# Optimization experiments

Measured on AMD Instinct MI355X. Metric: run time of the kernel, lower is better.

## Reference

```python
import jax, jax.numpy as jnp
import numpy as np

B, Hh, Ww, E = 8, 32, 32, 256
HEADS = 8
KD = E // HEADS  # 32
FFN = 1024
NQ = 64
SCALING = KD ** -0.5
EPS = 1e-6


def _ln(x, g, b):
    m = x.mean(-1, keepdims=True)
    v = ((x - m) ** 2).mean(-1, keepdims=True)
    return (x - m) * jax.lax.rsqrt(v + EPS) * g + b


def _dwconv(x, w, b, pad):
    # x: (b,h,w,c); w: (c,1,kh,kw) depthwise
    y = jnp.transpose(x, (0, 3, 1, 2))
    y = jax.lax.conv_general_dilated(
        y, w, (1, 1), [(pad, pad), (pad, pad)],
        dimension_numbers=('NCHW', 'OIHW', 'NCHW'),
        feature_group_count=y.shape[1])
    y = y + b[None, :, None, None]
    return jnp.transpose(y, (0, 2, 3, 1))


def _rot2(x):
    x1 = x[..., ::2]
    x2 = x[..., 1::2]
    return jnp.stack([-x2, x1], axis=-1).reshape(x.shape)


def _theta_shift(x, sin, cos):
    return x * cos + _rot2(x) * sin


def _ffn(x, fc1_w, fc1_b, fc2_w, fc2_b):
    h = jax.nn.gelu(x @ fc1_w.T + fc1_b, approximate=False)
    return h @ fc2_w.T + fc2_b


def _mha(q, k, v, in_w, in_b, out_w, out_b):
    # torch nn.MultiheadAttention, batch_first=True
    wq, wk, wv = in_w[:E], in_w[E:2 * E], in_w[2 * E:]
    bq, bk, bv = in_b[:E], in_b[E:2 * E], in_b[2 * E:]
    b_, nq, _ = q.shape
    lk = k.shape[1]
    qp = (q @ wq.T + bq).reshape(b_, nq, HEADS, KD).transpose(0, 2, 1, 3)
    kp = (k @ wk.T + bk).reshape(b_, lk, HEADS, KD).transpose(0, 2, 1, 3)
    vp = (v @ wv.T + bv).reshape(b_, lk, HEADS, KD).transpose(0, 2, 1, 3)
    att = jax.nn.softmax(jnp.einsum('bhqd,bhkd->bhqk', qp, kp) * SCALING, axis=-1)
    out = jnp.einsum('bhqk,bhkd->bhqd', att, vp)
    out = out.transpose(0, 2, 1, 3).reshape(b_, nq, E)
    return out @ out_w.T + out_b


def setup_inputs() -> dict:
    key = jax.random.key(0)
    ks = jax.random.split(key, 24)
    n = lambda i, shp, s=1.0: jax.random.normal(ks[i], shp, jnp.float32) * s
    W = 0.02
    return {
        'x': n(0, (B, Hh, Ww, E)),
        'queries': n(1, (B, NQ, E)),
        'sin': n(2, (Hh, Ww, KD)),
        'cos': n(3, (Hh, Ww, KD)),
        'mask': n(4, (HEADS, Hh * Ww, Hh * Ww)),
        'ln1_g': jnp.ones((E,), jnp.float32), 'ln1_b': jnp.zeros((E,), jnp.float32),
        'ln2_g': jnp.ones((E,), jnp.float32), 'ln2_b': jnp.zeros((E,), jnp.float32),
        'wq': n(5, (E, E), W), 'bq': jnp.zeros((E,), jnp.float32),
        'wk': n(6, (E, E), W), 'bk': jnp.zeros((E,), jnp.float32),
        'wv': n(7, (E, E), W), 'bv': jnp.zeros((E,), jnp.float32),
        'lepe_w': n(8, (E, 1, 5, 5), W), 'lepe_b': jnp.zeros((E,), jnp.float32),
        'wo': n(9, (E, E), W), 'bo': jnp.zeros((E,), jnp.float32),
        'fc1_w': n(10, (FFN, E), W), 'fc1_b': jnp.zeros((FFN,), jnp.float32),
        'fc2_w': n(11, (E, FFN), W), 'fc2_b': jnp.zeros((E,), jnp.float32),
        'pos_w': n(12, (E, 1, 3, 3), W), 'pos_b': jnp.zeros((E,), jnp.float32),
        'ca_in_w': n(13, (3 * E, E), W), 'ca_in_b': jnp.zeros((3 * E,), jnp.float32),
        'ca_out_w': n(14, (E, E), W), 'ca_out_b': jnp.zeros((E,), jnp.float32),
    }


def reference(x, queries, sin, cos, mask, ln1_g, ln1_b, ln2_g, ln2_b,
              wq, bq, wk, bk, wv, bv, lepe_w, lepe_b, wo, bo,
              fc1_w, fc1_b, fc2_w, fc2_b, pos_w, pos_b,
              ca_in_w, ca_in_b, ca_out_w, ca_out_b):
    # conditional positional encoding
    x = x + _dwconv(x, pos_w, pos_b, 1)

    # --- retention branch (VisionRetentionAll) ---
    hn = _ln(x, ln1_g, ln1_b)
    q = hn @ wq.T + bq
    k = (hn @ wk.T + bk) * SCALING
    v = hn @ wv.T + bv
    lepe = _dwconv(v, lepe_w, lepe_b, 2)
    b_, hh, ww, _ = x.shape
    L = hh * ww
    qh = q.reshape(b_, hh, ww, HEADS, KD).transpose(0, 3, 1, 2, 4)
    kh = k.reshape(b_, hh, ww, HEADS, KD).transpose(0, 3, 1, 2, 4)
    qr = _theta_shift(qh, sin, cos).reshape(b_, HEADS, L, KD)
    kr = _theta_shift(kh, sin, cos).reshape(b_, HEADS, L, KD)
    vr = v.reshape(b_, hh, ww, HEADS, KD).transpose(0, 3, 1, 2, 4).reshape(b_, HEADS, L, KD)
    att = jax.nn.softmax(jnp.einsum('bnqd,bnkd->bnqk', qr, kr) + mask, axis=-1)
    out = jnp.einsum('bnqk,bnkd->bnqd', att, vr)
    out = out.transpose(0, 2, 1, 3).reshape(b_, hh, ww, E) + lepe
    x = x + (out @ wo.T + bo)

    # --- FFN branch ---
    x = x + _ffn(_ln(x, ln2_g, ln2_b), fc1_w, fc1_b, fc2_w, fc2_b)

    # --- cross-attention on queries ---
    xs = x.reshape(b_, L, E)
    q_ln = _ln(queries, ln1_g, ln1_b)
    queries = queries + _mha(q_ln, xs, xs, ca_in_w, ca_in_b, ca_out_w, ca_out_b)
    queries = queries + _ffn(_ln(queries, ln2_g, ln2_b), fc1_w, fc1_b, fc2_w, fc2_b)
    return x, queries
```

## Files before the change

kernel.cpp:

```cpp
#include <hip/hip_runtime.h>
#include <hip/hip_bf16.h>

#define B_      8
#define HH      32
#define WW      32
#define E_      256
#define HEADS_  8
#define KD_     32
#define FFN_    1024
#define NQ_     64
#define L_      1024
#define SCALING_ 0.17677669529663687f
#define EPS_    1e-6f

typedef short bf16x8 __attribute__((ext_vector_type(8)));
typedef float f32x4 __attribute__((ext_vector_type(4)));
typedef unsigned short ushort_t;

__device__ __forceinline__ ushort_t f2bf(float f) {
    __hip_bfloat16 h = __float2bfloat16(f);
    return *reinterpret_cast<ushort_t*>(&h);
}
__device__ __forceinline__ float bf2f(ushort_t u) {
    __hip_bfloat16 h = *reinterpret_cast<__hip_bfloat16*>(&u);
    return __bfloat162float(h);
}

__global__ void dwT_kernel(const float* __restrict__ lepe_w, const float* __restrict__ pos_w,
                           float* __restrict__ LWT, float* __restrict__ PWT) {
    int e = threadIdx.x;
#pragma unroll
    for (int t = 0; t < 25; ++t) LWT[t * 256 + e] = lepe_w[e * 25 + t];
#pragma unroll
    for (int t = 0; t < 9; ++t) PWT[t * 256 + e] = pos_w[e * 9 + t];
}

__global__ __launch_bounds__(256) void posconv_ln2(
        const float* __restrict__ x, const float* __restrict__ PWT,
        const float* __restrict__ bias, const float* __restrict__ g,
        const float* __restrict__ bb, float* __restrict__ X, ushort_t* __restrict__ HN) {
    int tid = threadIdx.x;
    int wave = tid >> 6, lane = tid & 63;
    int b = blockIdx.x >> 8, rem = blockIdx.x & 255;
    int hh = rem >> 3, wg = rem & 7;
    int ww = wg * 4 + wave;
    int e = lane * 4;
    long row = ((long)(b * HH + hh)) * WW + ww;

    float4 bi = *reinterpret_cast<const float4*>(bias + e);
    float ax = bi.x, ay = bi.y, az = bi.z, aw = bi.w;
#pragma unroll
    for (int dh = 0; dh < 3; ++dh) {
        int h2 = hh + dh - 1; if (h2 < 0 || h2 >= HH) continue;
        float rx = 0.f, ry = 0.f, rz = 0.f, rw = 0.f;
#pragma unroll
        for (int dw = 0; dw < 3; ++dw) {
            int w2 = ww + dw - 1; if (w2 < 0 || w2 >= WW) continue;
            float4 v = *reinterpret_cast<const float4*>(x + (((long)(b * HH + h2)) * WW + w2) * E_ + e);
            float4 wt = *reinterpret_cast<const float4*>(PWT + (dh * 3 + dw) * 256 + e);
            rx += v.x * wt.x; ry += v.y * wt.y; rz += v.z * wt.z; rw += v.w * wt.w;
        }
        ax += rx; ay += ry; az += rz; aw += rw;
    }
    float4 x4 = *reinterpret_cast<const float4*>(x + row * E_ + e);
    float vx = x4.x + ax, vy = x4.y + ay, vz = x4.z + az, vw = x4.w + aw;
    float4 o4 = {vx, vy, vz, vw};
    *reinterpret_cast<float4*>(X + row * E_ + e) = o4;

    float s = vx + vy + vz + vw;
#pragma unroll
    for (int off = 1; off < 64; off <<= 1) s += __shfl_xor(s, off);
    float mean = s * (1.0f / E_);
    float dx = vx - mean, dy = vy - mean, dz = vz - mean, dw_ = vw - mean;
    float s2 = dx * dx + dy * dy + dz * dz + dw_ * dw_;
#pragma unroll
    for (int off = 1; off < 64; off <<= 1) s2 += __shfl_xor(s2, off);
    float r = rsqrtf(s2 * (1.0f / E_) + EPS_);
    float4 g4 = *reinterpret_cast<const float4*>(g + e);
    float4 b4 = *reinterpret_cast<const float4*>(bb + e);
    uint2 p;
    p.x = (unsigned int)f2bf(dx * r * g4.x + b4.x) | ((unsigned int)f2bf(dy * r * g4.y + b4.y) << 16);
    p.y = (unsigned int)f2bf(dz * r * g4.z + b4.z) | ((unsigned int)f2bf(dw_ * r * g4.w + b4.w) << 16);
    *reinterpret_cast<uint2*>(HN + row * E_ + e) = p;
}

__global__ __launch_bounds__(256) void lepe2(
        const float* __restrict__ v, const float* __restrict__ LWT,
        const float* __restrict__ bias, float* __restrict__ out) {
    int tid = threadIdx.x;
    int wave = tid >> 6, lane = tid & 63;
    int b = blockIdx.x >> 8, rem = blockIdx.x & 255;
    int hh = rem >> 3, wg = rem & 7;
    int ww = wg * 4 + wave;
    int e = lane * 4;
    long row = ((long)(b * HH + hh)) * WW + ww;

    float4 bi = *reinterpret_cast<const float4*>(bias + e);
    float ax = bi.x, ay = bi.y, az = bi.z, aw = bi.w;
#pragma unroll
    for (int dh = 0; dh < 5; ++dh) {
        int h2 = hh + dh - 2; if (h2 < 0 || h2 >= HH) continue;
        float rx = 0.f, ry = 0.f, rz = 0.f, rw = 0.f;
#pragma unroll
        for (int dw = 0; dw < 5; ++dw) {
            int w2 = ww + dw - 2; if (w2 < 0 || w2 >= WW) continue;
            float4 vv = *reinterpret_cast<const float4*>(v + (((long)(b * HH + h2)) * WW + w2) * E_ + e);
            float4 wt = *reinterpret_cast<const float4*>(LWT + (dh * 5 + dw) * 256 + e);
            rx += vv.x * wt.x; ry += vv.y * wt.y; rz += vv.z * wt.z; rw += vv.w * wt.w;
        }
        ax += rx; ay += ry; az += rz; aw += rw;
    }
    float4 o4 = {ax, ay, az, aw};
    *reinterpret_cast<float4*>(out + row * E_ + e) = o4;
}

__global__ __launch_bounds__(256) void ln2(
        const float* __restrict__ x, const float* __restrict__ g,
        const float* __restrict__ b, ushort_t* __restrict__ y) {
    int tid = threadIdx.x;
    int wave = tid >> 6, lane = tid & 63;
    long row = (long)blockIdx.x * 4 + wave;
    int e = lane * 4;
    float4 v4 = *reinterpret_cast<const float4*>(x + row * E_ + e);
    float s = v4.x + v4.y + v4.z + v4.w;
#pragma unroll
    for (int off = 1; off < 64; off <<= 1) s += __shfl_xor(s, off);
    float mean = s * (1.0f / E_);
    float dx = v4.x - mean, dy = v4.y - mean, dz = v4.z - mean, dw = v4.w - mean;
    float s2 = dx * dx + dy * dy + dz * dz + dw * dw;
#pragma unroll
    for (int off = 1; off < 64; off <<= 1) s2 += __shfl_xor(s2, off);
    float r = rsqrtf(s2 * (1.0f / E_) + EPS_);
    float4 g4 = *reinterpret_cast<const float4*>(g + e);
    float4 b4 = *reinterpret_cast<const float4*>(b + e);
    uint2 p;
    p.x = (unsigned int)f2bf(dx * r * g4.x + b4.x) | ((unsigned int)f2bf(dy * r * g4.y + b4.y) << 16);
    p.y = (unsigned int)f2bf(dz * r * g4.z + b4.z) | ((unsigned int)f2bf(dw * r * g4.w + b4.w) << 16);
    *reinterpret_cast<uint2*>(y + row * E_ + e) = p;
}

__global__ void maskcvt_kernel(const float* __restrict__ m, ushort_t* __restrict__ o) {
    long i = ((long)blockIdx.x * 256 + threadIdx.x) * 4;
    float4 v = *reinterpret_cast<const float4*>(m + i);
    uint2 p;
    p.x = (unsigned int)f2bf(v.x) | ((unsigned int)f2bf(v.y) << 16);
    p.y = (unsigned int)f2bf(v.z) | ((unsigned int)f2bf(v.w) << 16);
    *reinterpret_cast<uint2*>(o + i) = p;
}

struct WTab { const float* src[8]; };
__global__ void wconv_kernel(WTab t, ushort_t* __restrict__ dst) {
    const int off[9] = {0, 65536, 131072, 196608, 262144, 524288, 786432, 983040, 1048576};
    long base = ((long)blockIdx.x * 256 + threadIdx.x) * 4;
    int r = 0;
#pragma unroll
    for (int i = 1; i < 8; ++i) r = (base >= off[i]) ? i : r;
    const float* s =
        r == 0 ? t.src[0] : r == 1 ? t.src[1] : r == 2 ? t.src[2] : r == 3 ? t.src[3] :
        r == 4 ? t.src[4] : r == 5 ? t.src[5] : r == 6 ? t.src[6] : t.src[7];
    float4 v = *reinterpret_cast<const float4*>(s + (base - off[r]));
    uint2 p;
    p.x = (unsigned int)f2bf(v.x) | ((unsigned int)f2bf(v.y) << 16);
    p.y = (unsigned int)f2bf(v.z) | ((unsigned int)f2bf(v.w) << 16);
    *reinterpret_cast<uint2*>(dst + base) = p;
}

template<int ACT, int THETA>
__global__ __launch_bounds__(256) void gemm2(
        const ushort_t* __restrict__ A, const ushort_t* __restrict__ W,
        const float* __restrict__ bias, ushort_t* __restrict__ Cb,
        float* __restrict__ Cf, const float* __restrict__ resid,
        int M, int N, int K, float scale, int scaleN,
        const float* __restrict__ sinp, const float* __restrict__ cosp) {
    __shared__ __align__(16) ushort_t As[64 * 72];
    __shared__ __align__(16) ushort_t Ws[64 * 72];
    int tid = threadIdx.x;
    int wave = tid >> 6, lane = tid & 63;
    int quad = lane >> 4, l16 = lane & 15;
    int wm = wave >> 1, wn = wave & 1;
    long mBase = (long)blockIdx.x * 64;
    long nBase = (long)blockIdx.y * 64;
    int row = tid >> 3, q = tid & 7;
    int row2 = (tid + 256) >> 3, q2 = (tid + 256) & 7;

    f32x4 acc[2][2];
#pragma unroll
    for (int i = 0; i < 2; ++i)
#pragma unroll
        for (int j = 0; j < 2; ++j) acc[i][j] = (f32x4){0.f, 0.f, 0.f, 0.f};

    int nT = K >> 6;
    uint4 a0 = *reinterpret_cast<const uint4*>(A + (mBase + row) * (long)K + q * 8);
    uint4 a1 = *reinterpret_cast<const uint4*>(A + (mBase + row2) * (long)K + q2 * 8);
    uint4 w0 = *reinterpret_cast<const uint4*>(W + (nBase + row) * (long)K + q * 8);
    uint4 w1 = *reinterpret_cast<const uint4*>(W + (nBase + row2) * (long)K + q2 * 8);

    for (int t = 0; t < nT; ++t) {
        *reinterpret_cast<uint4*>(&As[row * 72 + q * 8]) = a0;
        *reinterpret_cast<uint4*>(&As[row2 * 72 + q2 * 8]) = a1;
        *reinterpret_cast<uint4*>(&Ws[row * 72 + q * 8]) = w0;
        *reinterpret_cast<uint4*>(&Ws[row2 * 72 + q2 * 8]) = w1;
        __syncthreads();
        if (t + 1 < nT) {
            int kt = (t + 1) << 6;
            a0 = *reinterpret_cast<const uint4*>(A + (mBase + row) * (long)K + kt + q * 8);
            a1 = *reinterpret_cast<const uint4*>(A + (mBase + row2) * (long)K + kt + q2 * 8);
            w0 = *reinterpret_cast<const uint4*>(W + (nBase + row) * (long)K + kt + q * 8);
            w1 = *reinterpret_cast<const uint4*>(W + (nBase + row2) * (long)K + kt + q2 * 8);
        }
#pragma unroll
        for (int kk = 0; kk < 2; ++kk) {
            bf16x8 af[2], bfr[2];
#pragma unroll
            for (int i = 0; i < 2; ++i)
                af[i] = *reinterpret_cast<const bf16x8*>(&As[(wm * 32 + i * 16 + l16) * 72 + kk * 32 + quad * 8]);
#pragma unroll
            for (int j = 0; j < 2; ++j)
                bfr[j] = *reinterpret_cast<const bf16x8*>(&Ws[(wn * 32 + j * 16 + l16) * 72 + kk * 32 + quad * 8]);
#pragma unroll
            for (int i = 0; i < 2; ++i)
#pragma unroll
                for (int j = 0; j < 2; ++j)
                    acc[i][j] = __builtin_amdgcn_mfma_f32_16x16x32_bf16(af[i], bfr[j], acc[i][j], 0, 0, 0);
        }
        __syncthreads();
    }

#pragma unroll
    for (int i = 0; i < 2; ++i)
#pragma unroll
        for (int j = 0; j < 2; ++j) {
            long n = nBase + wn * 32 + j * 16 + l16;
            float bn = bias[n];
            float eff = (n < scaleN) ? scale : 1.0f;
#pragma unroll
            for (int r = 0; r < 4; ++r) {
                long m = mBase + wm * 32 + i * 16 + quad * 4 + r;
                float v = (acc[i][j][r] + bn) * eff;
                if (THETA) {
                    float other = __shfl_xor(v, 1);
                    int l = (int)(m & (L_ - 1));
                    int d = (int)(n & 31);
                    float cc = cosp[l * 32 + d], ss = sinp[l * 32 + d];
                    v = v * cc + ((n & 1) ? other : -other) * ss;
                }
                if (ACT) v = 0.5f * v * (1.0f + erff(v * 0.70710678118654752f));
                if (resid) v += resid[m * N + n];
                if (Cf) Cf[m * N + n] = v;
                if (Cb) Cb[m * N + n] = f2bf(v);
            }
        }
}

__global__ __launch_bounds__(256) void attn3(
        const ushort_t* __restrict__ Q, int qs,
        const ushort_t* __restrict__ K, int ks,
        const ushort_t* __restrict__ V, int vs,
        const ushort_t* __restrict__ maskbf,
        const float* __restrict__ lepe, ushort_t* __restrict__ out, int nq) {
    __shared__ __align__(16) ushort_t Vt[2][32 * 136];
    __shared__ __align__(16) ushort_t Pl[4][16 * 136];
    int tid = threadIdx.x;
    int wave = tid >> 6, lane = tid & 63;
    int quad = lane >> 4, l16 = lane & 15;
    int qt = blockIdx.x, h = blockIdx.y, b = blockIdx.z;
    int qbase = qt * 64 + wave * 16;

    bf16x8 qfrag = *reinterpret_cast<const bf16x8*>(
        Q + ((long)b * nq + qbase + l16) * qs + h * KD_ + quad * 8);

    f32x4 acc_o[2];
    acc_o[0] = (f32x4){0.f, 0.f, 0.f, 0.f};
    acc_o[1] = (f32x4){0.f, 0.f, 0.f, 0.f};
    float lsum[4] = {0.f, 0.f, 0.f, 0.f};

    int kp = tid & 63;
    int dq = tid >> 6;

    const ushort_t* vp = V + ((long)b * L_ + 2 * kp) * vs + h * KD_ + dq * 8;
    uint4 ua = *reinterpret_cast<const uint4*>(vp);
    uint4 ub = *reinterpret_cast<const uint4*>(vp + vs);
    {
        const unsigned int* wa = reinterpret_cast<const unsigned int*>(&ua);
        const unsigned int* wb = reinterpret_cast<const unsigned int*>(&ub);
#pragma unroll
        for (int i = 0; i < 8; ++i) {
            unsigned int x16 = (wa[i >> 1] >> ((i & 1) * 16)) & 0xFFFF;
            unsigned int y16 = (wb[i >> 1] >> ((i & 1) * 16)) & 0xFFFF;
            *reinterpret_cast<unsigned int*>(&Vt[0][(dq * 8 + i) * 136 + 2 * kp]) =
                x16 | (y16 << 16);
        }
    }

    for (int it = 0; it < 8; ++it) {
        int kb = it * 128;
        __syncthreads();
        if (it < 7) {
            const ushort_t* vn = V + ((long)b * L_ + kb + 128 + 2 * kp) * vs + h * KD_ + dq * 8;
            ua = *reinterpret_cast<const uint4*>(vn);
            ub = *reinterpret_cast<const uint4*>(vn + vs);
        }

#pragma unroll
        for (int g = 0; g < 2; ++g) {
            bf16x8 kf[4];
#pragma unroll
            for (int kt = 0; kt < 4; ++kt)
                kf[kt] = *reinterpret_cast<const bf16x8*>(
                    K + ((long)b * L_ + kb + (g * 4 + kt) * 16 + l16) * ks + h * KD_ + quad * 8);
#pragma unroll
            for (int kt = 0; kt < 4; ++kt) {
                int kcol = (g * 4 + kt) * 16;
                f32x4 sa;
                if (maskbf) {
#pragma unroll
                    for (int r = 0; r < 4; ++r)
                        sa[r] = bf2f(maskbf[((long)h * L_ + qbase + quad * 4 + r) * L_ + kb + kcol + l16]);
                } else {
                    sa = (f32x4){0.f, 0.f, 0.f, 0.f};
                }
                sa = __builtin_amdgcn_mfma_f32_16x16x32_bf16(qfrag, kf[kt], sa, 0, 0, 0);
#pragma unroll
                for (int r = 0; r < 4; ++r) {
                    float p = __expf(sa[r]);
                    lsum[r] += p;
                    Pl[wave][(quad * 4 + r) * 136 + kcol + l16] = f2bf(p);
                }
            }
        }

#pragma unroll
        for (int c = 0; c < 4; ++c) {
            bf16x8 pa = *reinterpret_cast<const bf16x8*>(
                &Pl[wave][l16 * 136 + c * 32 + quad * 8]);
#pragma unroll
            for (int dt = 0; dt < 2; ++dt) {
                bf16x8 vf = *reinterpret_cast<const bf16x8*>(
                    &Vt[it & 1][(dt * 16 + l16) * 136 + c * 32 + quad * 8]);
                acc_o[dt] = __builtin_amdgcn_mfma_f32_16x16x32_bf16(pa, vf, acc_o[dt], 0, 0, 0);
            }
        }

        if (it < 7) {
            const unsigned int* wa = reinterpret_cast<const unsigned int*>(&ua);
            const unsigned int* wb = reinterpret_cast<const unsigned int*>(&ub);
#pragma unroll
            for (int i = 0; i < 8; ++i) {
                unsigned int x16 = (wa[i >> 1] >> ((i & 1) * 16)) & 0xFFFF;
                unsigned int y16 = (wb[i >> 1] >> ((i & 1) * 16)) & 0xFFFF;
                *reinterpret_cast<unsigned int*>(&Vt[(it + 1) & 1][(dq * 8 + i) * 136 + 2 * kp]) =
                    x16 | (y16 << 16);
            }
        }
    }

#pragma unroll
    for (int off = 1; off < 16; off <<= 1) {
#pragma unroll
        for (int r = 0; r < 4; ++r) lsum[r] += __shfl_xor(lsum[r], off);
    }

#pragma unroll
    for (int dt = 0; dt < 2; ++dt)
#pragma unroll
        for (int r = 0; r < 4; ++r) {
            float v = acc_o[dt][r] / lsum[r];
            long oi = ((long)b * nq + qbase + quad * 4 + r) * E_ + h * KD_ + dt * 16 + l16;
            if (lepe) v += lepe[oi];
            out[oi] = f2bf(v);
        }
}

extern "C" void kernel_launch(void* const* d_in, const int* in_sizes, int n_in,
                              void* d_out, int out_size, void* d_ws, size_t ws_size,
                              hipStream_t stream) {
    const float* x        = (const float*)d_in[0];
    const float* queries  = (const float*)d_in[1];
    const float* sinp     = (const float*)d_in[2];
    const float* cosp     = (const float*)d_in[3];
    const float* mask     = (const float*)d_in[4];
    const float* ln1_g    = (const float*)d_in[5];
    const float* ln1_b    = (const float*)d_in[6];
    const float* ln2_g    = (const float*)d_in[7];
    const float* ln2_b    = (const float*)d_in[8];
    const float* wq       = (const float*)d_in[9];
    const float* bq       = (const float*)d_in[10];
    const float* wk       = (const float*)d_in[11];
    const float* bk       = (const float*)d_in[12];
    const float* wv       = (const float*)d_in[13];
    const float* bv       = (const float*)d_in[14];
    const float* lepe_w   = (const float*)d_in[15];
    const float* lepe_b   = (const float*)d_in[16];
    const float* wo       = (const float*)d_in[17];
    const float* bo       = (const float*)d_in[18];
    const float* fc1_w    = (const float*)d_in[19];
    const float* fc1_b    = (const float*)d_in[20];
    const float* fc2_w    = (const float*)d_in[21];
    const float* fc2_b    = (const float*)d_in[22];
    const float* pos_w    = (const float*)d_in[23];
    const float* pos_b    = (const float*)d_in[24];
    const float* ca_in_w  = (const float*)d_in[25];
    const float* ca_in_b  = (const float*)d_in[26];
    const float* ca_out_w = (const float*)d_in[27];
    const float* ca_out_b = (const float*)d_in[28];

    float* ws = (float*)d_ws;
    const long SZ = (long)B_ * L_ * E_;
    float* X    = ws;
    float* Vbf  = ws + SZ;
    float* LEP  = ws + 2 * SZ;
    float* Q2   = LEP;
    ushort_t* U = (ushort_t*)(ws + 3 * SZ);
    ushort_t* T0    = U;
    ushort_t* Qb_u  = U + SZ;
    ushort_t* Kb_u  = U + 2 * SZ;
    ushort_t* Vb_u  = U + 3 * SZ;
    ushort_t* HID_u = U + 4 * SZ;
    ushort_t* MB_u  = HID_u;
    ushort_t* WB    = U + 8 * SZ;
    float* LWT      = (float*)(WB + 1048576);
    float* PWT      = LWT + 6400;
    ushort_t* KV_u   = U + SZ;
    ushort_t* QLN_u  = Vb_u;
    ushort_t* QP_u   = Vb_u + 131072;
    ushort_t* CAO_u  = Vb_u + 262144;
    ushort_t* QHID_u = Vb_u + 393216;
    ushort_t* wqB    = WB;
    ushort_t* wkB    = WB + 65536;
    ushort_t* wvB    = WB + 131072;
    ushort_t* woB    = WB + 196608;
    ushort_t* fc1B   = WB + 262144;
    ushort_t* fc2B   = WB + 524288;
    ushort_t* cainB  = WB + 786432;
    ushort_t* caoutB = WB + 983040;

    float* XOUT = (float*)d_out;
    float* QOUT = (float*)d_out + 2097152;

    dim3 blk(256);
    const int rows = B_ * L_;
    const float* Z = nullptr;

    WTab wt;
    wt.src[0] = wq; wt.src[1] = wk; wt.src[2] = wv; wt.src[3] = wo;
    wt.src[4] = fc1_w; wt.src[5] = fc2_w; wt.src[6] = ca_in_w; wt.src[7] = ca_out_w;

    dwT_kernel<<<1, blk, 0, stream>>>(lepe_w, pos_w, LWT, PWT);
    wconv_kernel<<<1024, blk, 0, stream>>>(wt, WB);
    maskcvt_kernel<<<8192, blk, 0, stream>>>(mask, MB_u);
    posconv_ln2<<<2048, blk, 0, stream>>>(x, PWT, pos_b, ln1_g, ln1_b, X, T0);

    gemm2<0,1><<<dim3(128, 4), blk, 0, stream>>>(T0, wqB, bq, Qb_u, nullptr, Z, rows, 256, 256, 1.0f, 0, sinp, cosp);
    gemm2<0,1><<<dim3(128, 4), blk, 0, stream>>>(T0, wkB, bk, Kb_u, nullptr, Z, rows, 256, 256, SCALING_, 256, sinp, cosp);
    gemm2<0,0><<<dim3(128, 4), blk, 0, stream>>>(T0, wvB, bv, Vb_u, Vbf, Z, rows, 256, 256, 1.0f, 0, Z, Z);
    lepe2<<<2048, blk, 0, stream>>>(Vbf, LWT, lepe_b, LEP);
    attn3<<<dim3(16, 8, 8), blk, 0, stream>>>(Qb_u, 256, Kb_u, 256, Vb_u, 256, MB_u, LEP, T0, L_);
    gemm2<0,0><<<dim3(128, 4), blk, 0, stream>>>(T0, woB, bo, nullptr, X, X, rows, 256, 256, 1.0f, 0, Z, Z);
    ln2<<<2048, blk, 0, stream>>>(X, ln2_g, ln2_b, T0);
    gemm2<1,0><<<dim3(128, 16), blk, 0, stream>>>(T0, fc1B, fc1_b, HID_u, nullptr, Z, rows, 1024, 256, 1.0f, 0, Z, Z);
    gemm2<0,0><<<dim3(128, 4), blk, 0, stream>>>(HID_u, fc2B, fc2_b, T0, XOUT, X, rows, 256, 1024, 1.0f, 0, Z, Z);

    ln2<<<128, blk, 0, stream>>>(queries, ln1_g, ln1_b, QLN_u);
    gemm2<0,0><<<dim3(8, 4), blk, 0, stream>>>(QLN_u, cainB, ca_in_b, QP_u, nullptr, Z, 512, 256, 256, 1.0f, 0, Z, Z);
    gemm2<0,0><<<dim3(128, 8), blk, 0, stream>>>(T0, cainB + 65536, ca_in_b + 256, KV_u, nullptr, Z, rows, 512, 256, SCALING_, 256, Z, Z);
    attn3<<<dim3(1, 8, 8), blk, 0, stream>>>(QP_u, 256, KV_u, 512, KV_u + 256, 512, nullptr, nullptr, CAO_u, NQ_);
    gemm2<0,0><<<dim3(8, 4), blk, 0, stream>>>(CAO_u, caoutB, ca_out_b, nullptr, Q2, queries, 512, 256, 256, 1.0f, 0, Z, Z);
    ln2<<<128, blk, 0, stream>>>(Q2, ln2_g, ln2_b, QLN_u);
    gemm2<1,0><<<dim3(8, 16), blk, 0, stream>>>(QLN_u, fc1B, fc1_b, QHID_u, nullptr, Z, 512, 1024, 256, 1.0f, 0, Z, Z);
    gemm2<0,0><<<dim3(8, 4), blk, 0, stream>>>(QHID_u, fc2B, fc2_b, nullptr, QOUT, Q2, 512, 256, 1024, 1.0f, 0, Z, Z);
}
```

Before: 367.3 us.

## Fold log2e into K scale and mask, use exp2 and transposed score MFMA

The log2(e) factor is folded into the key scaling and the bf16 mask conversion, so softmax can use the native exp2 instead of expf. The score MFMA swaps its operands, so each lane holds four consecutive keys of one query row. This allows vectorized mask loads preloaded into registers, packed bf16 stores of P to LDS, and a single running sum per lane reduced with fewer shuffles. Float-to-bf16 packing also moves to a paired conversion helper everywhere. The mask now stores pre-scaled values, which changes bf16 rounding slightly and raises register use for the preloaded mask.

```diff
diff --git a/kernel.cpp b/kernel.cpp
--- a/kernel.cpp
+++ b/kernel.cpp
@@ -11,19 +11,26 @@
 #define NQ_     64
 #define L_      1024
 #define SCALING_ 0.17677669529663687f
+#define LOG2E_  1.44269504088896340736f
 #define EPS_    1e-6f
 
 typedef short bf16x8 __attribute__((ext_vector_type(8)));
 typedef float f32x4 __attribute__((ext_vector_type(4)));
 typedef unsigned short ushort_t;
 
+#if __has_builtin(__builtin_amdgcn_exp2f)
+#define EXP2(x) __builtin_amdgcn_exp2f(x)
+#else
+#define EXP2(x) exp2f(x)
+#endif
+
 __device__ __forceinline__ ushort_t f2bf(float f) {
     __hip_bfloat16 h = __float2bfloat16(f);
     return *reinterpret_cast<ushort_t*>(&h);
 }
-__device__ __forceinline__ float bf2f(ushort_t u) {
-    __hip_bfloat16 h = *reinterpret_cast<__hip_bfloat16*>(&u);
-    return __bfloat162float(h);
+__device__ __forceinline__ unsigned int pk2(float a, float b) {
+    __hip_bfloat162 h = __float22bfloat162_rn(float2{a, b});
+    return *reinterpret_cast<unsigned int*>(&h);
 }
 
 __global__ void dwT_kernel(const float* __restrict__ lepe_w, const float* __restrict__ pos_w,
@@ -79,8 +86,8 @@
     float4 g4 = *reinterpret_cast<const float4*>(g + e);
     float4 b4 = *reinterpret_cast<const float4*>(bb + e);
     uint2 p;
-    p.x = (unsigned int)f2bf(dx * r * g4.x + b4.x) | ((unsigned int)f2bf(dy * r * g4.y + b4.y) << 16);
-    p.y = (unsigned int)f2bf(dz * r * g4.z + b4.z) | ((unsigned int)f2bf(dw_ * r * g4.w + b4.w) << 16);
+    p.x = pk2(dx * r * g4.x + b4.x, dy * r * g4.y + b4.y);
+    p.y = pk2(dz * r * g4.z + b4.z, dw_ * r * g4.w + b4.w);
     *reinterpret_cast<uint2*>(HN + row * E_ + e) = p;
 }
 
@@ -134,8 +141,8 @@
     float4 g4 = *reinterpret_cast<const float4*>(g + e);
     float4 b4 = *reinterpret_cast<const float4*>(b + e);
     uint2 p;
-    p.x = (unsigned int)f2bf(dx * r * g4.x + b4.x) | ((unsigned int)f2bf(dy * r * g4.y + b4.y) << 16);
-    p.y = (unsigned int)f2bf(dz * r * g4.z + b4.z) | ((unsigned int)f2bf(dw * r * g4.w + b4.w) << 16);
+    p.x = pk2(dx * r * g4.x + b4.x, dy * r * g4.y + b4.y);
+    p.y = pk2(dz * r * g4.z + b4.z, dw * r * g4.w + b4.w);
     *reinterpret_cast<uint2*>(y + row * E_ + e) = p;
 }
 
@@ -143,8 +150,8 @@
     long i = ((long)blockIdx.x * 256 + threadIdx.x) * 4;
     float4 v = *reinterpret_cast<const float4*>(m + i);
     uint2 p;
-    p.x = (unsigned int)f2bf(v.x) | ((unsigned int)f2bf(v.y) << 16);
-    p.y = (unsigned int)f2bf(v.z) | ((unsigned int)f2bf(v.w) << 16);
+    p.x = pk2(v.x * LOG2E_, v.y * LOG2E_);
+    p.y = pk2(v.z * LOG2E_, v.w * LOG2E_);
     *reinterpret_cast<uint2*>(o + i) = p;
 }
 
@@ -160,8 +167,8 @@
         r == 4 ? t.src[4] : r == 5 ? t.src[5] : r == 6 ? t.src[6] : t.src[7];
     float4 v = *reinterpret_cast<const float4*>(s + (base - off[r]));
     uint2 p;
-    p.x = (unsigned int)f2bf(v.x) | ((unsigned int)f2bf(v.y) << 16);
-    p.y = (unsigned int)f2bf(v.z) | ((unsigned int)f2bf(v.w) << 16);
+    p.x = pk2(v.x, v.y);
+    p.y = pk2(v.z, v.w);
     *reinterpret_cast<uint2*>(dst + base) = p;
 }
 
@@ -252,7 +259,7 @@
         }
 }
 
-__global__ __launch_bounds__(256) void attn3(
+__global__ __launch_bounds__(256) void attn4(
         const ushort_t* __restrict__ Q, int qs,
         const ushort_t* __restrict__ K, int ks,
         const ushort_t* __restrict__ V, int vs,
@@ -272,7 +279,7 @@
     f32x4 acc_o[2];
     acc_o[0] = (f32x4){0.f, 0.f, 0.f, 0.f};
     acc_o[1] = (f32x4){0.f, 0.f, 0.f, 0.f};
-    float lsum[4] = {0.f, 0.f, 0.f, 0.f};
+    float lsum = 0.f;
 
     int kp = tid & 63;
     int dq = tid >> 6;
@@ -300,32 +307,39 @@
             ua = *reinterpret_cast<const uint4*>(vn);
             ub = *reinterpret_cast<const uint4*>(vn + vs);
         }
+        uint2 mreg[8];
+        if (maskbf) {
+            const ushort_t* mb = maskbf + ((long)h * L_ + qbase + l16) * L_ + kb + quad * 4;
+#pragma unroll
+            for (int kt = 0; kt < 8; ++kt)
+                mreg[kt] = *reinterpret_cast<const uint2*>(mb + kt * 16);
+        }
 
 #pragma unroll
         for (int g = 0; g < 2; ++g) {
             bf16x8 kf[4];
 #pragma unroll
-            for (int kt = 0; kt < 4; ++kt)
-                kf[kt] = *reinterpret_cast<const bf16x8*>(
-                    K + ((long)b * L_ + kb + (g * 4 + kt) * 16 + l16) * ks + h * KD_ + quad * 8);
-#pragma unroll
-            for (int kt = 0; kt < 4; ++kt) {
-                int kcol = (g * 4 + kt) * 16;
-                f32x4 sa;
+            for (int kt4 = 0; kt4 < 4; ++kt4)
+                kf[kt4] = *reinterpret_cast<const bf16x8*>(
+                    K + ((long)b * L_ + kb + (g * 4 + kt4) * 16 + l16) * ks + h * KD_ + quad * 8);
+#pragma unroll
+            for (int kt4 = 0; kt4 < 4; ++kt4) {
+                int kt = g * 4 + kt4;
+                f32x4 sa = (f32x4){0.f, 0.f, 0.f, 0.f};
+                sa = __builtin_amdgcn_mfma_f32_16x16x32_bf16(kf[kt4], qfrag, sa, 0, 0, 0);
+                float s0 = sa[0], s1 = sa[1], s2 = sa[2], s3 = sa[3];
                 if (maskbf) {
-#pragma unroll
-                    for (int r = 0; r < 4; ++r)
-                        sa[r] = bf2f(maskbf[((long)h * L_ + qbase + quad * 4 + r) * L_ + kb + kcol + l16]);
-                } else {
-                    sa = (f32x4){0.f, 0.f, 0.f, 0.f};
+                    s0 += __uint_as_float(mreg[kt].x << 16);
+                    s1 += __uint_as_float(mreg[kt].x & 0xFFFF0000u);
+                    s2 += __uint_as_float(mreg[kt].y << 16);
+                    s3 += __uint_as_float(mreg[kt].y & 0xFFFF0000u);
                 }
-                sa = __builtin_amdgcn_mfma_f32_16x16x32_bf16(qfrag, kf[kt], sa, 0, 0, 0);
-#pragma unroll
-                for (int r = 0; r < 4; ++r) {
-                    float p = __expf(sa[r]);
-                    lsum[r] += p;
-                    Pl[wave][(quad * 4 + r) * 136 + kcol + l16] = f2bf(p);
-                }
+                float p0 = EXP2(s0), p1 = EXP2(s1), p2 = EXP2(s2), p3 = EXP2(s3);
+                lsum += (p0 + p1) + (p2 + p3);
+                uint2 pw;
+                pw.x = pk2(p0, p1);
+                pw.y = pk2(p2, p3);
+                *reinterpret_cast<uint2*>(&Pl[wave][l16 * 136 + kt * 16 + quad * 4]) = pw;
             }
         }
 
@@ -354,17 +368,17 @@
         }
     }
 
-#pragma unroll
-    for (int off = 1; off < 16; off <<= 1) {
-#pragma unroll
-        for (int r = 0; r < 4; ++r) lsum[r] += __shfl_xor(lsum[r], off);
-    }
+    lsum += __shfl_xor(lsum, 16);
+    lsum += __shfl_xor(lsum, 32);
+    float ls[4];
+#pragma unroll
+    for (int r = 0; r < 4; ++r) ls[r] = __shfl(lsum, quad * 4 + r);
 
 #pragma unroll
     for (int dt = 0; dt < 2; ++dt)
 #pragma unroll
         for (int r = 0; r < 4; ++r) {
-            float v = acc_o[dt][r] / lsum[r];
+            float v = acc_o[dt][r] / ls[r];
             long oi = ((long)b * nq + qbase + quad * 4 + r) * E_ + h * KD_ + dt * 16 + l16;
             if (lepe) v += lepe[oi];
             out[oi] = f2bf(v);
@@ -440,6 +454,7 @@
     dim3 blk(256);
     const int rows = B_ * L_;
     const float* Z = nullptr;
+    const float KSCL = SCALING_ * LOG2E_;
 
     WTab wt;
     wt.src[0] = wq; wt.src[1] = wk; wt.src[2] = wv; wt.src[3] = wo;
@@ -451,10 +466,10 @@
     posconv_ln2<<<2048, blk, 0, stream>>>(x, PWT, pos_b, ln1_g, ln1_b, X, T0);
 
     gemm2<0,1><<<dim3(128, 4), blk, 0, stream>>>(T0, wqB, bq, Qb_u, nullptr, Z, rows, 256, 256, 1.0f, 0, sinp, cosp);
-    gemm2<0,1><<<dim3(128, 4), blk, 0, stream>>>(T0, wkB, bk, Kb_u, nullptr, Z, rows, 256, 256, SCALING_, 256, sinp, cosp);
+    gemm2<0,1><<<dim3(128, 4), blk, 0, stream>>>(T0, wkB, bk, Kb_u, nullptr, Z, rows, 256, 256, KSCL, 256, sinp, cosp);
     gemm2<0,0><<<dim3(128, 4), blk, 0, stream>>>(T0, wvB, bv, Vb_u, Vbf, Z, rows, 256, 256, 1.0f, 0, Z, Z);
     lepe2<<<2048, blk, 0, stream>>>(Vbf, LWT, lepe_b, LEP);
-    attn3<<<dim3(16, 8, 8), blk, 0, stream>>>(Qb_u, 256, Kb_u, 256, Vb_u, 256, MB_u, LEP, T0, L_);
+    attn4<<<dim3(16, 8, 8), blk, 0, stream>>>(Qb_u, 256, Kb_u, 256, Vb_u, 256, MB_u, LEP, T0, L_);
     gemm2<0,0><<<dim3(128, 4), blk, 0, stream>>>(T0, woB, bo, nullptr, X, X, rows, 256, 256, 1.0f, 0, Z, Z);
     ln2<<<2048, blk, 0, stream>>>(X, ln2_g, ln2_b, T0);
     gemm2<1,0><<<dim3(128, 16), blk, 0, stream>>>(T0, fc1B, fc1_b, HID_u, nullptr, Z, rows, 1024, 256, 1.0f, 0, Z, Z);
@@ -462,8 +477,8 @@
 
     ln2<<<128, blk, 0, stream>>>(queries, ln1_g, ln1_b, QLN_u);
     gemm2<0,0><<<dim3(8, 4), blk, 0, stream>>>(QLN_u, cainB, ca_in_b, QP_u, nullptr, Z, 512, 256, 256, 1.0f, 0, Z, Z);
-    gemm2<0,0><<<dim3(128, 8), blk, 0, stream>>>(T0, cainB + 65536, ca_in_b + 256, KV_u, nullptr, Z, rows, 512, 256, SCALING_, 256, Z, Z);
-    attn3<<<dim3(1, 8, 8), blk, 0, stream>>>(QP_u, 256, KV_u, 512, KV_u + 256, 512, nullptr, nullptr, CAO_u, NQ_);
+    gemm2<0,0><<<dim3(128, 8), blk, 0, stream>>>(T0, cainB + 65536, ca_in_b + 256, KV_u, nullptr, Z, rows, 512, 256, KSCL, 256, Z, Z);
+    attn4<<<dim3(1, 8, 8), blk, 0, stream>>>(QP_u, 256, KV_u, 512, KV_u + 256, 512, nullptr, nullptr, CAO_u, NQ_);
     gemm2<0,0><<<dim3(8, 4), blk, 0, stream>>>(CAO_u, caoutB, ca_out_b, nullptr, Q2, queries, 512, 256, 256, 1.0f, 0, Z, Z);
     ln2<<<128, blk, 0, stream>>>(Q2, ln2_g, ln2_b, QLN_u);
     gemm2<1,0><<<dim3(8, 16), blk, 0, stream>>>(QLN_u, fc1B, fc1_b, QHID_u, nullptr, Z, 512, 1024, 256, 1.0f, 0, Z, Z);
```

Measured after the change: 371.5 us. About the same (+1.1%).
